# Optimization experiments

Hardware: AMD Instinct MI355X
Metric: run time of the kernel (lower is better)

Reference implementation:

```python
import jax, jax.numpy as jnp
import numpy as np

EMBED_DIM = 1024
NUM_HEADS = 16
HEAD_DIM = EMBED_DIM // NUM_HEADS
B, L = 4, 2048


def setup_inputs() -> dict:
    key = jax.random.key(0)
    k1, k2, k3 = jax.random.split(key, 3)
    s = 1.0 / np.sqrt(EMBED_DIM)
    x = jax.random.normal(k1, (B, L, EMBED_DIM), dtype=jnp.float32)
    w_qkv = jax.random.normal(k2, (EMBED_DIM, 3 * EMBED_DIM), dtype=jnp.float32) * s
    b_qkv = jnp.zeros((3 * EMBED_DIM,), dtype=jnp.float32)
    w_out = jax.random.normal(k3, (EMBED_DIM, EMBED_DIM), dtype=jnp.float32) * s
    b_out = jnp.zeros((EMBED_DIM,), dtype=jnp.float32)
    return {"x": x, "w_qkv": w_qkv, "b_qkv": b_qkv, "w_out": w_out, "b_out": b_out}


def reference(x, w_qkv, b_qkv, w_out, b_out):
    Bb, Ll, _ = x.shape
    scale = HEAD_DIM ** -0.5
    qkv = x @ w_qkv + b_qkv                      # [B, L, 3E]
    qkv = qkv.reshape(Bb, Ll, 3, NUM_HEADS, HEAD_DIM)
    q, k, v = qkv[:, :, 0], qkv[:, :, 1], qkv[:, :, 2]   # [B, L, H, D]
    # scores: [B, H, L, L]
    scores = jnp.einsum("bqhd,bkhd->bhqk", q, k) * scale
    causal = jnp.tril(jnp.ones((Ll, Ll), dtype=bool))     # True = keep
    scores = jnp.where(causal, scores, jnp.float32(-1e9))
    attn_probs = jax.nn.softmax(scores, axis=-1)
    context = jnp.einsum("bhqk,bkhd->bqhd", attn_probs, v)
    context = context.reshape(Bb, Ll, EMBED_DIM)
    out = context @ w_out + b_out
    return (out, attn_probs)
```

## Files before the change

### kernel.cpp

```cpp
#include <hip/hip_runtime.h>


typedef __attribute__((ext_vector_type(8))) short short8;
typedef __attribute__((ext_vector_type(4))) short short4v;
typedef __attribute__((ext_vector_type(4))) float f32x4;
typedef __attribute__((ext_vector_type(2))) unsigned int u32x2;

#define MFMA_BF16(a,b,c) __builtin_amdgcn_mfma_f32_16x16x32_bf16((a),(b),(c),0,0,0)

#define GLDS(gp, lp) __builtin_amdgcn_global_load_lds( \
    (const __attribute__((address_space(1))) unsigned int*)(gp), \
    (__attribute__((address_space(3))) unsigned int*)(lp), 16, 0, 0)

__device__ __forceinline__ unsigned short f2bf(float f) {
    union { float f; unsigned u; } v; v.f = f;
    return (unsigned short)((v.u + 0x7FFFu + ((v.u >> 16) & 1u)) >> 16);
}

#define QK_SCALE 0.18033688011112042f

__global__ __launch_bounds__(256) void k_cast(const float* __restrict__ src,
                                              unsigned short* __restrict__ dst, int n8) {
    int i = blockIdx.x * 256 + threadIdx.x;
    if (i >= n8) return;
    const float4* s = (const float4*)src + (size_t)i * 2;
    float4 a = s[0], b = s[1];
    short8 o;
    o[0] = f2bf(a.x); o[1] = f2bf(a.y); o[2] = f2bf(a.z); o[3] = f2bf(a.w);
    o[4] = f2bf(b.x); o[5] = f2bf(b.y); o[6] = f2bf(b.z); o[7] = f2bf(b.w);
    ((short8*)dst)[i] = o;
}

__global__ __launch_bounds__(256) void k_transpose_cast(const float* __restrict__ src,
                                                        unsigned short* __restrict__ dst,
                                                        int R, int C) {
    __shared__ unsigned short t[64][72];
    int c0 = blockIdx.x * 64, r0 = blockIdx.y * 64;
    int tid = threadIdx.x;
    int rl = tid >> 2, cs = (tid & 3) * 16;
    const float* sp = src + (size_t)(r0 + rl) * C + c0 + cs;
    #pragma unroll
    for (int j = 0; j < 16; j += 4) {
        float4 v = *(const float4*)(sp + j);
        t[rl][cs + j + 0] = f2bf(v.x);
        t[rl][cs + j + 1] = f2bf(v.y);
        t[rl][cs + j + 2] = f2bf(v.z);
        t[rl][cs + j + 3] = f2bf(v.w);
    }
    __syncthreads();
    int clq = tid >> 2, rs = (tid & 3) * 16;
    short8 o0, o1;
    #pragma unroll
    for (int j = 0; j < 8; ++j) o0[j] = (short)t[rs + j][clq];
    #pragma unroll
    for (int j = 0; j < 8; ++j) o1[j] = (short)t[rs + 8 + j][clq];
    unsigned short* dp = dst + (size_t)(c0 + clq) * R + r0 + rs;
    *(short8*)dp = o0;
    *(short8*)(dp + 8) = o1;
}

__global__ __launch_bounds__(256) void k_gemm_qkv(
    const unsigned short* __restrict__ A,
    const unsigned short* __restrict__ Bt,
    const float* __restrict__ bias,
    unsigned short* __restrict__ qb,
    unsigned short* __restrict__ kb,
    unsigned short* __restrict__ vb)
{
    __shared__ unsigned short As[128 * 32];
    __shared__ unsigned short Bs[128 * 32];
    const int m0 = blockIdx.y * 128, n0 = blockIdx.x * 128;
    const int tid = threadIdx.x, w = tid >> 6, l = tid & 63;
    const int wm = w >> 1, wn = w & 1;
    const int g = l >> 4, cl = l & 15;
    const int srow = w * 16 + (l >> 2);
    const int soff = (l & 3) * 8;
    f32x4 acc[4][4] = {};

    for (int k0 = 0; k0 < 1024; k0 += 32) {
        __syncthreads();
        #pragma unroll
        for (int c = 0; c < 2; ++c) {
            GLDS(A  + (size_t)(m0 + c * 64 + srow) * 1024 + k0 + soff, &As[(c * 64 + w * 16) * 32]);
            GLDS(Bt + (size_t)(n0 + c * 64 + srow) * 1024 + k0 + soff, &Bs[(c * 64 + w * 16) * 32]);
        }
        __syncthreads();
        short8 af[4], bfr[4];
        #pragma unroll
        for (int i = 0; i < 4; ++i) af[i]  = *(const short8*)&As[(wm * 64 + i * 16 + cl) * 32 + g * 8];
        #pragma unroll
        for (int i = 0; i < 4; ++i) bfr[i] = *(const short8*)&Bs[(wn * 64 + i * 16 + cl) * 32 + g * 8];
        #pragma unroll
        for (int mi = 0; mi < 4; ++mi)
            #pragma unroll
            for (int ni = 0; ni < 4; ++ni)
                acc[mi][ni] = MFMA_BF16(af[mi], bfr[ni], acc[mi][ni]);
    }
    #pragma unroll
    for (int ni = 0; ni < 4; ++ni) {
        int col = n0 + wn * 64 + ni * 16 + cl;
        int which = col >> 10, h = (col >> 6) & 15, d = col & 63;
        unsigned short* dst = which == 0 ? qb : (which == 1 ? kb : vb);
        float bv = bias[col];
        float sc = (which == 0) ? QK_SCALE : 1.0f;
        #pragma unroll
        for (int mi = 0; mi < 4; ++mi) {
            #pragma unroll
            for (int i = 0; i < 4; ++i) {
                int row = m0 + wm * 64 + mi * 16 + g * 4 + i;
                int b = row >> 11, ll = row & 2047;
                dst[((size_t)(b * 16 + h) * 2048 + ll) * 64 + d] = f2bf((acc[mi][ni][i] + bv) * sc);
            }
        }
    }
}

__global__ __launch_bounds__(256) void k_gemm_out(
    const unsigned short* __restrict__ A,
    const unsigned short* __restrict__ Bt,
    const float* __restrict__ bias,
    float* __restrict__ out)
{
    __shared__ unsigned short As[128 * 32];
    __shared__ unsigned short Bs[128 * 32];
    const int m0 = blockIdx.y * 128, n0 = blockIdx.x * 128;
    const int tid = threadIdx.x, w = tid >> 6, l = tid & 63;
    const int wm = w >> 1, wn = w & 1;
    const int g = l >> 4, cl = l & 15;
    const int srow = w * 16 + (l >> 2);
    const int soff = (l & 3) * 8;
    f32x4 acc[4][4] = {};

    for (int k0 = 0; k0 < 1024; k0 += 32) {
        __syncthreads();
        #pragma unroll
        for (int c = 0; c < 2; ++c) {
            GLDS(A  + (size_t)(m0 + c * 64 + srow) * 1024 + k0 + soff, &As[(c * 64 + w * 16) * 32]);
            GLDS(Bt + (size_t)(n0 + c * 64 + srow) * 1024 + k0 + soff, &Bs[(c * 64 + w * 16) * 32]);
        }
        __syncthreads();
        short8 af[4], bfr[4];
        #pragma unroll
        for (int i = 0; i < 4; ++i) af[i]  = *(const short8*)&As[(wm * 64 + i * 16 + cl) * 32 + g * 8];
        #pragma unroll
        for (int i = 0; i < 4; ++i) bfr[i] = *(const short8*)&Bs[(wn * 64 + i * 16 + cl) * 32 + g * 8];
        #pragma unroll
        for (int mi = 0; mi < 4; ++mi)
            #pragma unroll
            for (int ni = 0; ni < 4; ++ni)
                acc[mi][ni] = MFMA_BF16(af[mi], bfr[ni], acc[mi][ni]);
    }
    #pragma unroll
    for (int ni = 0; ni < 4; ++ni) {
        int col = n0 + wn * 64 + ni * 16 + cl;
        float bv = bias[col];
        #pragma unroll
        for (int mi = 0; mi < 4; ++mi) {
            #pragma unroll
            for (int i = 0; i < 4; ++i) {
                int row = m0 + wm * 64 + mi * 16 + g * 4 + i;
                out[(size_t)row * 1024 + col] = acc[mi][ni][i] + bv;
            }
        }
    }
}

__device__ __forceinline__ void stage_qk(const unsigned short* gbase,
                                         unsigned short* lds, int w, int l) {
    const int lr = l >> 3;
    const int lc = (l & 7) ^ lr;
    #pragma unroll
    for (int c = 0; c < 2; ++c) {
        const int r0 = (w * 2 + c) * 8;
        GLDS(gbase + (size_t)(r0 + lr) * 64 + (lc << 3), lds + r0 * 64);
    }
}

__global__ __launch_bounds__(256, 4) void k_attn(
    const unsigned short* __restrict__ qb,
    const unsigned short* __restrict__ kb,
    const unsigned short* __restrict__ vb,
    float* __restrict__ probs,
    unsigned short* __restrict__ ctx)
{
    __shared__ unsigned short Ks[2][64 * 64];
    __shared__ unsigned short Vt[2][64 * 64];
    __shared__ unsigned short Ps[4 * 16 * 64];

    const int lid = blockIdx.y * 32 + blockIdx.x;
    const int nl  = (lid & 7) * 256 + (lid >> 3);
    const int qt  = 31 - (nl & 31);
    const int bh  = nl >> 5;

    const int tid = threadIdx.x;
    const int w = tid >> 6, l = tid & 63;
    const int g = l >> 4, cl = l & 15;

    const unsigned short* Qg = qb + (size_t)bh * (2048 * 64);
    const unsigned short* Kg = kb + (size_t)bh * (2048 * 64);
    const unsigned short* Vg = vb + (size_t)bh * (2048 * 64);

    stage_qk(Qg + (size_t)qt * (64 * 64), Vt[0], w, l);
    stage_qk(Kg, Ks[0], w, l);
    __syncthreads();

    const int qr = w * 16 + cl;
    short8 aq0 = *(const short8*)&Vt[0][qr * 64 + ((g ^ (qr & 7)) << 3)];
    short8 aq1 = *(const short8*)&Vt[0][qr * 64 + (((g + 4) ^ (qr & 7)) << 3)];

    float lpart = 0.f;
    for (int kt = 0; kt <= qt; ++kt) {
        const unsigned short* K = Ks[kt & 1];
        if (kt < qt) {
            stage_qk(Kg + (size_t)(kt + 1) * (64 * 64), Ks[(kt & 1) ^ 1], w, l);
            #pragma unroll
            for (int kf = 0; kf < 4; ++kf) {
                int r = kf * 16 + cl;
                short8 b0 = *(const short8*)&K[r * 64 + ((g ^ (r & 7)) << 3)];
                short8 b1 = *(const short8*)&K[r * 64 + (((g + 4) ^ (r & 7)) << 3)];
                f32x4 acc = {0.f, 0.f, 0.f, 0.f};
                acc = MFMA_BF16(b0, aq0, acc);
                acc = MFMA_BF16(b1, aq1, acc);
                #pragma unroll
                for (int i = 0; i < 4; ++i)
                    lpart += __builtin_amdgcn_exp2f(acc[i]);
            }
        } else {
            #pragma unroll
            for (int kf = 0; kf < 4; ++kf) {
                int r = kf * 16 + cl;
                short8 b0 = *(const short8*)&K[r * 64 + ((g ^ (r & 7)) << 3)];
                short8 b1 = *(const short8*)&K[r * 64 + (((g + 4) ^ (r & 7)) << 3)];
                f32x4 acc = {0.f, 0.f, 0.f, 0.f};
                acc = MFMA_BF16(b0, aq0, acc);
                acc = MFMA_BF16(b1, aq1, acc);
                #pragma unroll
                for (int i = 0; i < 4; ++i) {
                    float e = __builtin_amdgcn_exp2f(acc[i]);
                    lpart += ((kf * 16 + g * 4 + i) > qr) ? 0.f : e;
                }
            }
        }
        __syncthreads();
    }

    float lr;
    {
        float s = lpart;
        s += __shfl_xor(s, 16);
        s += __shfl_xor(s, 32);
        lr = -__log2f(s);
    }

    stage_qk(Kg, Ks[0], w, l);
    const int vkp = tid & 31;
    const int vd0 = (tid >> 5) * 8;
    short8 va  = *(const short8*)(Vg + (size_t)(2 * vkp) * 64 + vd0);
    short8 vb8 = *(const short8*)(Vg + (size_t)(2 * vkp + 1) * 64 + vd0);

    f32x4 cacc[4] = {};
    const size_t prow = ((size_t)bh * 2048 + qt * 64 + qr) * 2048;

    for (int kt = 0; kt <= qt; ++kt) {
        const int cur = kt & 1;
        const bool last = (kt == qt);

        unsigned int* VtW = (unsigned int*)Vt[cur];
        #pragma unroll
        for (int j = 0; j < 8; ++j) {
            unsigned int pk = (unsigned int)(unsigned short)va[j]
                            | ((unsigned int)(unsigned short)vb8[j] << 16);
            VtW[(vd0 + j) * 32 + (((vkp >> 2) ^ j) << 2) + (vkp & 3)] = pk;
        }
        if (!last) {
            va  = *(const short8*)(Vg + (size_t)((kt + 1) * 64 + 2 * vkp) * 64 + vd0);
            vb8 = *(const short8*)(Vg + (size_t)((kt + 1) * 64 + 2 * vkp + 1) * 64 + vd0);
        }
        __syncthreads();

        if (!last) stage_qk(Kg + (size_t)(kt + 1) * (64 * 64), Ks[cur ^ 1], w, l);

        const unsigned short* K = Ks[cur];
        #pragma unroll
        for (int kf = 0; kf < 4; ++kf) {
            int r = kf * 16 + cl;
            short8 b0 = *(const short8*)&K[r * 64 + ((g ^ (r & 7)) << 3)];
            short8 b1 = *(const short8*)&K[r * 64 + (((g + 4) ^ (r & 7)) << 3)];
            f32x4 acc = {0.f, 0.f, 0.f, 0.f};
            acc = MFMA_BF16(b0, aq0, acc);
            acc = MFMA_BF16(b1, aq1, acc);
            f32x4 p4;
            #pragma unroll
            for (int i = 0; i < 4; ++i) {
                float p = __builtin_amdgcn_exp2f(acc[i] + lr);
                if (last && (kf * 16 + g * 4 + i) > qr) p = 0.f;
                p4[i] = p;
            }
            *(f32x4*)&probs[prow + kt * 64 + kf * 16 + g * 4] = p4;
            u32x2 uq;
            uq[0] = (unsigned)f2bf(p4[0]) | ((unsigned)f2bf(p4[1]) << 16);
            uq[1] = (unsigned)f2bf(p4[2]) | ((unsigned)f2bf(p4[3]) << 16);
            int e0 = (kf * 16 + g * 4) ^ ((cl & 7) << 3);
            *(u32x2*)&Ps[(w * 16 + cl) * 64 + e0] = uq;
        }

        #pragma unroll
        for (int ks = 0; ks < 2; ++ks) {
            int er = (ks * 32 + g * 8) ^ ((cl & 7) << 3);
            short8 paf = *(const short8*)&Ps[(w * 16 + cl) * 64 + er];
            #pragma unroll
            for (int df = 0; df < 4; ++df) {
                int vr = df * 16 + cl;
                short8 vf = *(const short8*)&Vt[cur][vr * 64 + (((ks * 4 + g) ^ (vr & 7)) << 3)];
                cacc[df] = MFMA_BF16(vf, paf, cacc[df]);
            }
        }
    }

    {
        const int b = bh >> 4, h = bh & 15;
        const size_t crow = ((size_t)(b * 2048 + qt * 64 + qr)) * 1024 + h * 64;
        #pragma unroll
        for (int df = 0; df < 4; ++df) {
            short4v cv;
            #pragma unroll
            for (int i = 0; i < 4; ++i) cv[i] = (short)f2bf(cacc[df][i]);
            *(short4v*)&ctx[crow + df * 16 + g * 4] = cv;
        }
    }

    {
        const int col0 = (qt + 1) * 64;
        if (col0 < 2048) {
            const f32x4 z = {0.f, 0.f, 0.f, 0.f};
            float* tp = probs + ((size_t)bh * 2048 + qt * 64) * 2048;
            for (int r = 0; r < 64; ++r) {
                float* rp = tp + (size_t)r * 2048;
                for (int cc = col0 + tid * 4; cc < 2048; cc += 1024)
                    __builtin_nontemporal_store(z, (f32x4*)&rp[cc]);
            }
        }
    }
}

extern "C" void kernel_launch(void* const* d_in, const int* in_sizes, int n_in,
                              void* d_out, int out_size, void* d_ws, size_t ws_size,
                              hipStream_t stream) {
    const float* x     = (const float*)d_in[0];
    const float* w_qkv = (const float*)d_in[1];
    const float* b_qkv = (const float*)d_in[2];
    const float* w_out = (const float*)d_in[3];
    const float* b_out = (const float*)d_in[4];

    float* out   = (float*)d_out;
    float* probs = out + (size_t)8192 * 1024;

    char* ws = (char*)d_ws;
    unsigned short* xb    = (unsigned short*)(ws);
    unsigned short* wqkvT = (unsigned short*)(ws + 16777216);
    unsigned short* woutT = (unsigned short*)(ws + 23068672);
    unsigned short* qb    = (unsigned short*)(ws + 25165824);
    unsigned short* kb    = (unsigned short*)(ws + 41943040);
    unsigned short* vb    = (unsigned short*)(ws + 58720256);
    unsigned short* ctx   = xb;

    k_cast<<<4096, 256, 0, stream>>>(x, xb, 1048576);
    k_transpose_cast<<<dim3(48, 16), 256, 0, stream>>>(w_qkv, wqkvT, 1024, 3072);
    k_transpose_cast<<<dim3(16, 16), 256, 0, stream>>>(w_out, woutT, 1024, 1024);
    k_gemm_qkv<<<dim3(24, 64), 256, 0, stream>>>(xb, wqkvT, b_qkv, qb, kb, vb);
    k_attn<<<dim3(32, 64), 256, 0, stream>>>(qb, kb, vb, probs, ctx);
    k_gemm_out<<<dim3(8, 64), 256, 0, stream>>>(ctx, woutT, b_out, out);
}
```

Measured before the change: 388.0 us.

## Move causal zero-fill into QKV GEMM launch and single-buffer V in attention

The upper-triangle zero stores for attn_probs move out of the attention kernel into extra blocks of the QKV GEMM grid, each of which handles a pair of query tiles to balance the work. The zero-fill traffic then overlaps with the compute-bound GEMM instead of the tail of attention. Attention also replaces the double-buffered V tile with one shared Q/V buffer and raises its blocks-per-SM hint from 4 to 5 to improve occupancy. The price is an extra barrier per key tile, and the GEMM's zero-fill blocks take CUs away from the GEMM blocks.

Measured after the change: 427.4 us. 10.1% more time.

```diff
diff --git a/kernel.cpp b/kernel.cpp
--- a/kernel.cpp
+++ b/kernel.cpp
@@ -65,8 +65,29 @@
     const float* __restrict__ bias,
     unsigned short* __restrict__ qb,
     unsigned short* __restrict__ kb,
-    unsigned short* __restrict__ vb)
+    unsigned short* __restrict__ vb,
+    float* __restrict__ probs)
 {
+    if (blockIdx.x >= 24) {
+        const int c = blockIdx.x - 24;
+        const int bh = blockIdx.y;
+        const int tid = threadIdx.x;
+        const f32x4 z = {0.f, 0.f, 0.f, 0.f};
+        #pragma unroll
+        for (int u = 0; u < 2; ++u) {
+            const int tt = u == 0 ? c : 31 - c;
+            const int col0 = (tt + 1) * 64;
+            if (col0 >= 2048) continue;
+            float* tp = probs + ((size_t)bh * 2048 + tt * 64) * 2048;
+            for (int r = 0; r < 64; ++r) {
+                float* rp = tp + (size_t)r * 2048;
+                for (int cc = col0 + tid * 4; cc < 2048; cc += 1024)
+                    __builtin_nontemporal_store(z, (f32x4*)&rp[cc]);
+            }
+        }
+        return;
+    }
+
     __shared__ unsigned short As[128 * 32];
     __shared__ unsigned short Bs[128 * 32];
     const int m0 = blockIdx.y * 128, n0 = blockIdx.x * 128;
@@ -176,7 +197,7 @@
     }
 }
 
-__global__ __launch_bounds__(256, 4) void k_attn(
+__global__ __launch_bounds__(256, 5) void k_attn(
     const unsigned short* __restrict__ qb,
     const unsigned short* __restrict__ kb,
     const unsigned short* __restrict__ vb,
@@ -184,7 +205,7 @@
     unsigned short* __restrict__ ctx)
 {
     __shared__ unsigned short Ks[2][64 * 64];
-    __shared__ unsigned short Vt[2][64 * 64];
+    __shared__ unsigned short QV[64 * 64];
     __shared__ unsigned short Ps[4 * 16 * 64];
 
     const int lid = blockIdx.y * 32 + blockIdx.x;
@@ -200,13 +221,13 @@
     const unsigned short* Kg = kb + (size_t)bh * (2048 * 64);
     const unsigned short* Vg = vb + (size_t)bh * (2048 * 64);
 
-    stage_qk(Qg + (size_t)qt * (64 * 64), Vt[0], w, l);
+    stage_qk(Qg + (size_t)qt * (64 * 64), QV, w, l);
     stage_qk(Kg, Ks[0], w, l);
     __syncthreads();
 
     const int qr = w * 16 + cl;
-    short8 aq0 = *(const short8*)&Vt[0][qr * 64 + ((g ^ (qr & 7)) << 3)];
-    short8 aq1 = *(const short8*)&Vt[0][qr * 64 + (((g + 4) ^ (qr & 7)) << 3)];
+    short8 aq0 = *(const short8*)&QV[qr * 64 + ((g ^ (qr & 7)) << 3)];
+    short8 aq1 = *(const short8*)&QV[qr * 64 + (((g + 4) ^ (qr & 7)) << 3)];
 
     float lpart = 0.f;
     for (int kt = 0; kt <= qt; ++kt) {
@@ -260,12 +281,14 @@
 
     f32x4 cacc[4] = {};
     const size_t prow = ((size_t)bh * 2048 + qt * 64 + qr) * 2048;
+    unsigned int* VtW = (unsigned int*)QV;
 
     for (int kt = 0; kt <= qt; ++kt) {
         const int cur = kt & 1;
         const bool last = (kt == qt);
 
-        unsigned int* VtW = (unsigned int*)Vt[cur];
+        __syncthreads();
+
         #pragma unroll
         for (int j = 0; j < 8; ++j) {
             unsigned int pk = (unsigned int)(unsigned short)va[j]
@@ -275,10 +298,9 @@
         if (!last) {
             va  = *(const short8*)(Vg + (size_t)((kt + 1) * 64 + 2 * vkp) * 64 + vd0);
             vb8 = *(const short8*)(Vg + (size_t)((kt + 1) * 64 + 2 * vkp + 1) * 64 + vd0);
-        }
-        __syncthreads();
-
-        if (!last) stage_qk(Kg + (size_t)(kt + 1) * (64 * 64), Ks[cur ^ 1], w, l);
+            stage_qk(Kg + (size_t)(kt + 1) * (64 * 64), Ks[cur ^ 1], w, l);
+        }
+        __syncthreads();
 
         const unsigned short* K = Ks[cur];
         #pragma unroll
@@ -311,7 +333,7 @@
             #pragma unroll
             for (int df = 0; df < 4; ++df) {
                 int vr = df * 16 + cl;
-                short8 vf = *(const short8*)&Vt[cur][vr * 64 + (((ks * 4 + g) ^ (vr & 7)) << 3)];
+                short8 vf = *(const short8*)&QV[vr * 64 + (((ks * 4 + g) ^ (vr & 7)) << 3)];
                 cacc[df] = MFMA_BF16(vf, paf, cacc[df]);
             }
         }
@@ -326,19 +348,6 @@
             #pragma unroll
             for (int i = 0; i < 4; ++i) cv[i] = (short)f2bf(cacc[df][i]);
             *(short4v*)&ctx[crow + df * 16 + g * 4] = cv;
-        }
-    }
-
-    {
-        const int col0 = (qt + 1) * 64;
-        if (col0 < 2048) {
-            const f32x4 z = {0.f, 0.f, 0.f, 0.f};
-            float* tp = probs + ((size_t)bh * 2048 + qt * 64) * 2048;
-            for (int r = 0; r < 64; ++r) {
-                float* rp = tp + (size_t)r * 2048;
-                for (int cc = col0 + tid * 4; cc < 2048; cc += 1024)
-                    __builtin_nontemporal_store(z, (f32x4*)&rp[cc]);
-            }
         }
     }
 }
@@ -367,7 +376,7 @@
     k_cast<<<4096, 256, 0, stream>>>(x, xb, 1048576);
     k_transpose_cast<<<dim3(48, 16), 256, 0, stream>>>(w_qkv, wqkvT, 1024, 3072);
     k_transpose_cast<<<dim3(16, 16), 256, 0, stream>>>(w_out, woutT, 1024, 1024);
-    k_gemm_qkv<<<dim3(24, 64), 256, 0, stream>>>(xb, wqkvT, b_qkv, qb, kb, vb);
+    k_gemm_qkv<<<dim3(40, 64), 256, 0, stream>>>(xb, wqkvT, b_qkv, qb, kb, vb, probs);
     k_attn<<<dim3(32, 64), 256, 0, stream>>>(qb, kb, vb, probs, ctx);
     k_gemm_out<<<dim3(8, 64), 256, 0, stream>>>(ctx, woutT, b_out, out);
 }
```
